# Kernel tuning notes

Measured on AMD Instinct MI355X. Metric: run time of the kernel, lower is better.

## Reference

```python
import jax, jax.numpy as jnp
import numpy as np

B, H, W, C = 2, 128, 128, 128
NS = 8                      # attn_num_splits
WH, WW = H // NS, W // NS   # window size 16x16
SH, SW = WH // 2, WW // 2   # shift sizes
HID = 2 * C * 4             # ffn hidden (in_channels = 2*d_model, expansion 4)
EPS = 1e-5


def _make_swin_mask():
    # Standard shifted-window attention mask: -100 between different regions.
    img = np.zeros((H, W), np.int32)
    cnt = 0
    for hs in (slice(0, -WH), slice(-WH, -SH), slice(-SH, None)):
        for ws in (slice(0, -WW), slice(-WW, -SW), slice(-SW, None)):
            img[hs, ws] = cnt
            cnt += 1
    ids = img.reshape(NS, WH, NS, WW).transpose(0, 2, 1, 3).reshape(NS * NS, WH * WW)
    mask = np.where(ids[:, None, :] != ids[:, :, None], -100.0, 0.0).astype(np.float32)
    return jnp.asarray(mask)  # (64, 256, 256)


def _layernorm(x, g, b):
    m = jnp.mean(x, axis=-1, keepdims=True)
    v = jnp.mean(jnp.square(x - m), axis=-1, keepdims=True)
    return (x - m) * jax.lax.rsqrt(v + EPS) * g + b


def setup_inputs() -> dict:
    key = jax.random.key(0)
    ks = jax.random.split(key, 8)
    s = 1.0 / np.sqrt(C)
    return {
        "source": jax.random.normal(ks[0], (B, H * W, C), jnp.float32),
        "target": jax.random.normal(ks[1], (B, H * W, C), jnp.float32),
        "Wq": jax.random.normal(ks[2], (C, C), jnp.float32) * s,
        "Wk": jax.random.normal(ks[3], (C, C), jnp.float32) * s,
        "Wv": jax.random.normal(ks[4], (C, C), jnp.float32) * s,
        "Wm": jax.random.normal(ks[5], (C, C), jnp.float32) * s,
        "g1": jnp.ones((C,), jnp.float32),
        "b1": jnp.zeros((C,), jnp.float32),
        "W1": jax.random.normal(ks[6], (2 * C, HID), jnp.float32) * (1.0 / np.sqrt(2 * C)),
        "W2": jax.random.normal(ks[7], (HID, C), jnp.float32) * (1.0 / np.sqrt(HID)),
        "g2": jnp.ones((C,), jnp.float32),
        "b2": jnp.zeros((C,), jnp.float32),
        "shifted_window_attn_mask": _make_swin_mask(),
        "height": H,
        "width": W,
        "attn_num_splits": NS,
    }


def reference(source, target, Wq, Wk, Wv, Wm, g1, b1, W1, W2, g2, b2,
              shifted_window_attn_mask, height, width, attn_num_splits):
    b, L, c = source.shape
    h, w, ns = height, width, attn_num_splits
    wh, ww = h // ns, w // ns
    sh, sw = wh // 2, ww // 2

    q = source @ Wq
    k = target @ Wk
    v = target @ Wv

    def to_windows(x):
        # (b, h*w, c) -> shifted -> (b, nWin, wh*ww, c)
        x = x.reshape(b, h, w, c)
        x = jnp.roll(x, (-sh, -sw), axis=(1, 2))
        x = x.reshape(b, ns, wh, ns, ww, c).transpose(0, 1, 3, 2, 4, 5)
        return x.reshape(b, ns * ns, wh * ww, c)

    qw, kw, vw = to_windows(q), to_windows(k), to_windows(v)
    scores = jnp.einsum('bnlc,bnmc->bnlm', qw, kw) / (c ** 0.5)
    scores = scores + shifted_window_attn_mask[None]  # broadcast over batch
    attn = jax.nn.softmax(scores, axis=-1)
    out = jnp.einsum('bnlm,bnmc->bnlc', attn, vw)

    # merge windows back and undo the shift
    out = out.reshape(b, ns, ns, wh, ww, c).transpose(0, 1, 3, 2, 4, 5).reshape(b, h, w, c)
    out = jnp.roll(out, (sh, sw), axis=(1, 2)).reshape(b, h * w, c)

    message = _layernorm(out @ Wm, g1, b1)
    ffn_in = jnp.concatenate([source, message], axis=-1)
    message = jax.nn.gelu(ffn_in @ W1, approximate=False) @ W2
    message = _layernorm(message, g2, b2)
    return source + message
```

## Files before the change

### kernel.cpp

```cpp
#include <hip/hip_runtime.h>
#include <math.h>
#include <stdint.h>


typedef unsigned short u16;
typedef __attribute__((ext_vector_type(8))) short bf16x8;
typedef __attribute__((ext_vector_type(4))) float f32x4;
typedef __attribute__((ext_vector_type(4))) short u16x4;
typedef __attribute__((ext_vector_type(2))) unsigned int u32x2;

__device__ __forceinline__ u16 f2b(float f) {
    unsigned int i = __float_as_uint(f);
    unsigned int r = (i + 0x7fffu + ((i >> 16) & 1u)) >> 16;
    return (u16)r;
}

__device__ __forceinline__ float gelu_e(float x) {
    float y = fabsf(x) * 0.70710678118f;
    float u = fmaf(y, fmaf(y, fmaf(y, fmaf(y, 0.078108f, 0.000972f),
                                   0.230389f), 0.278393f), 1.0f);
    u = u * u; u = u * u;
    float r = __builtin_amdgcn_rcpf(u);
    return fmaxf(x, 0.f) - 0.5f * fabsf(x) * r;
}

__device__ __forceinline__ void cp16(const void* g, void* l) {
    auto* gp = reinterpret_cast<const __attribute__((address_space(1))) unsigned int*>(
        reinterpret_cast<uintptr_t>(g));
    auto* lp = reinterpret_cast<__attribute__((address_space(3))) unsigned int*>(
        reinterpret_cast<uintptr_t>(l));
    __builtin_amdgcn_global_load_lds(gp, lp, 16, 0, 0);
}

__device__ __forceinline__ int win_map(int gm) {
    int b = gm >> 14, rr = gm & 16383;
    int win = rr >> 8, t = rr & 255;
    int wi = win >> 3, wj = win & 7, i = t >> 4, j = t & 15;
    int h = (wi * 16 + i + 8) & 127;
    int w = (wj * 16 + j + 8) & 127;
    return (b << 14) + h * 128 + w;
}

__global__ __launch_bounds__(256, 2)
void gemm_qkv(const u16* __restrict__ srcb, const u16* __restrict__ tgtb,
              const u16* __restrict__ Bt, u16* __restrict__ qw,
              u16* __restrict__ kw, u16* __restrict__ vwt)
{
    __shared__ __align__(16) u16 SMEM[32768];
    u16* As = SMEM;
    u16* Bs = SMEM + 16384;
    u16* Ts = SMEM;

    const int tid = threadIdx.x;
    const int w = tid >> 6, lane = tid & 63;
    const int lm = lane & 15, q = lane >> 4;
    const int wm = w >> 1, wn = w & 1;
    const int m0 = blockIdx.x * 128;
    const int y = blockIdx.y;
    const u16* Ab = (y == 0) ? srcb : tgtb;

#pragma unroll
    for (int s = 0; s < 4; ++s)
#pragma unroll
        for (int i = 0; i < 2; ++i) {
            int row = w * 32 + i * 16 + (lane >> 2);
            int kc = s * 32 + (lane & 3) * 8;
            cp16(Ab + (size_t)win_map(m0 + row) * 128 + kc,
                 (void*)(As + (s * 128 + w * 32 + i * 16) * 32));
            cp16(Bt + (size_t)(y * 128 + row) * 128 + kc,
                 (void*)(Bs + (s * 128 + w * 32 + i * 16) * 32));
        }
    __syncthreads();

    f32x4 acc[4][4] = {};
#pragma unroll
    for (int s = 0; s < 4; ++s) {
        bf16x8 af[4], bfr[4];
#pragma unroll
        for (int t = 0; t < 4; ++t)
            af[t] = *(const bf16x8*)(As + (s * 128 + wm * 64 + t * 16 + lm) * 32 + q * 8);
#pragma unroll
        for (int t = 0; t < 4; ++t)
            bfr[t] = *(const bf16x8*)(Bs + (s * 128 + wn * 64 + t * 16 + lm) * 32 + q * 8);
#pragma unroll
        for (int mt = 0; mt < 4; ++mt)
#pragma unroll
            for (int nt = 0; nt < 4; ++nt)
                acc[mt][nt] = __builtin_amdgcn_mfma_f32_16x16x32_bf16(
                    af[mt], bfr[nt], acc[mt][nt], 0, 0, 0);
    }

    __syncthreads();
#pragma unroll
    for (int mt = 0; mt < 4; ++mt)
#pragma unroll
        for (int nt = 0; nt < 4; ++nt)
#pragma unroll
            for (int r = 0; r < 4; ++r) {
                int rowl = wm * 64 + mt * 16 + q * 4 + r;
                int col = wn * 64 + nt * 16 + lm;
                int idx = (y == 2) ? col * 136 + rowl : rowl * 136 + col;
                Ts[idx] = f2b(acc[mt][nt][r]);
            }
    __syncthreads();
    const int c8 = (tid & 15) * 8;
#pragma unroll
    for (int i = 0; i < 8; ++i) {
        int rr = i * 16 + (tid >> 4);
        bf16x8 t = *(const bf16x8*)(Ts + rr * 136 + c8);
        if (y == 2) {
            int wix = m0 >> 8, tok0 = m0 & 255;
            *(bf16x8*)(vwt + (size_t)wix * 32768 + (size_t)rr * 256 + tok0 + c8) = t;
        } else {
            u16* Cv = (y == 0) ? qw : kw;
            *(bf16x8*)(Cv + (size_t)(m0 + rr) * 128 + c8) = t;
        }
    }
}

__global__ __launch_bounds__(256, 2)
void attn_msg(const u16* __restrict__ qw, const u16* __restrict__ kw,
              const u16* __restrict__ vt, const u16* __restrict__ wmt,
              const float* __restrict__ g, const float* __restrict__ bb,
              u16* __restrict__ msgb)
{
    __shared__ __align__(16) u16 Ps[64 * 264];
    __shared__ __align__(16) u16 B32[16384];

    const int tid = threadIdx.x, w = tid >> 6, lane = tid & 63;
    const int lm = lane & 15, q = lane >> 4;
    const int l4r = lane >> 2, l4c = (lane & 3) * 8;
    const int bid = blockIdx.x;
    const int qc = bid & 3, win = (bid >> 2) & 63, b = bid >> 8;
    const int wi = win >> 3, wj = win & 7;
    const int q0 = qc * 64;
    const size_t wbase = (size_t)(b * 64 + win);
    const u16* kwb = kw + wbase * 256 * 128;
    const u16* qwb = qw + wbase * 256 * 128;
    const u16* vtb = vt + wbase * 128 * 256;

    u16* Qs = Ps;
#pragma unroll
    for (int i = 0; i < 4; ++i)
        cp16(qwb + (size_t)(q0 + w * 16 + l4r) * 128 + i * 32 + l4c,
             (void*)(Qs + (i * 64 + w * 16) * 32));
#pragma unroll
    for (int s = 0; s < 4; ++s)
#pragma unroll
        for (int i = 0; i < 2; ++i) {
            int tok = w * 32 + i * 16 + l4r;
            cp16(kwb + (size_t)tok * 128 + s * 32 + l4c,
                 (void*)(B32 + (s * 128 + w * 32 + i * 16) * 32));
        }
    __syncthreads();

    bf16x8 af[4];
#pragma unroll
    for (int kt = 0; kt < 4; ++kt)
        af[kt] = *(const bf16x8*)(Qs + (kt * 64 + w * 16 + lm) * 32 + q * 8);

    f32x4 s[16];
#pragma unroll
    for (int nt = 0; nt < 16; ++nt) { f32x4 z = {0.f, 0.f, 0.f, 0.f}; s[nt] = z; }
#pragma unroll
    for (int kt = 0; kt < 4; ++kt)
#pragma unroll
        for (int nt = 0; nt < 8; ++nt) {
            bf16x8 bf = *(const bf16x8*)(B32 + (kt * 128 + nt * 16 + lm) * 32 + q * 8);
            s[nt] = __builtin_amdgcn_mfma_f32_16x16x32_bf16(af[kt], bf, s[nt], 0, 0, 0);
        }
    __syncthreads();
#pragma unroll
    for (int ss = 0; ss < 4; ++ss)
#pragma unroll
        for (int i = 0; i < 2; ++i) {
            int tok = 128 + w * 32 + i * 16 + l4r;
            cp16(kwb + (size_t)tok * 128 + ss * 32 + l4c,
                 (void*)(B32 + (ss * 128 + w * 32 + i * 16) * 32));
        }
    __syncthreads();
#pragma unroll
    for (int kt = 0; kt < 4; ++kt)
#pragma unroll
        for (int nt = 8; nt < 16; ++nt) {
            bf16x8 bf = *(const bf16x8*)(B32 + (kt * 128 + (nt - 8) * 16 + lm) * 32 + q * 8);
            s[nt] = __builtin_amdgcn_mfma_f32_16x16x32_bf16(af[kt], bf, s[nt], 0, 0, 0);
        }
    __syncthreads();

#pragma unroll
    for (int tt = 0; tt < 4; ++tt)
#pragma unroll
        for (int i = 0; i < 2; ++i) {
            int ch = w * 32 + i * 16 + l4r;
            cp16(vtb + (size_t)ch * 256 + tt * 32 + l4c,
                 (void*)(B32 + (tt * 128 + w * 32 + i * 16) * 32));
        }

    int idk[16];
#pragma unroll
    for (int nt = 0; nt < 16; ++nt) {
        int rh = (wi == 7) ? ((nt >= 8) ? 2 : 1) : 0;
        int rw = (wj == 7) ? ((lm >= 8) ? 2 : 1) : 0;
        idk[nt] = rh * 3 + rw;
    }
    const float scale = 0.08838834764831845f;
#pragma unroll
    for (int r = 0; r < 4; ++r) {
        int tq = q0 + w * 16 + q * 4 + r;
        int iq = tq >> 4, jq = tq & 15;
        int rhq = (wi == 7) ? ((iq >= 8) ? 2 : 1) : 0;
        int rwq = (wj == 7) ? ((jq >= 8) ? 2 : 1) : 0;
        int idq = rhq * 3 + rwq;
        float sv[16];
        float mx = -1e30f;
#pragma unroll
        for (int nt = 0; nt < 16; ++nt) {
            float x = s[nt][r] * scale + ((idq != idk[nt]) ? -100.f : 0.f);
            sv[nt] = x; mx = fmaxf(mx, x);
        }
        mx = fmaxf(mx, __shfl_xor(mx, 1));
        mx = fmaxf(mx, __shfl_xor(mx, 2));
        mx = fmaxf(mx, __shfl_xor(mx, 4));
        mx = fmaxf(mx, __shfl_xor(mx, 8));
        float sum = 0.f;
#pragma unroll
        for (int nt = 0; nt < 16; ++nt) { float e = __expf(sv[nt] - mx); sv[nt] = e; sum += e; }
        sum += __shfl_xor(sum, 1);
        sum += __shfl_xor(sum, 2);
        sum += __shfl_xor(sum, 4);
        sum += __shfl_xor(sum, 8);
        float inv = 1.0f / sum;
#pragma unroll
        for (int nt = 0; nt < 16; ++nt)
            Ps[(w * 16 + q * 4 + r) * 264 + nt * 16 + lm] = f2b(sv[nt] * inv);
    }
    __syncthreads();

    f32x4 o[8];
#pragma unroll
    for (int nt = 0; nt < 8; ++nt) { f32x4 z = {0.f, 0.f, 0.f, 0.f}; o[nt] = z; }
#pragma unroll
    for (int tt = 0; tt < 4; ++tt) {
        bf16x8 pf = *(const bf16x8*)(Ps + (w * 16 + lm) * 264 + tt * 32 + q * 8);
#pragma unroll
        for (int nt = 0; nt < 8; ++nt) {
            bf16x8 vf = *(const bf16x8*)(B32 + (tt * 128 + nt * 16 + lm) * 32 + q * 8);
            o[nt] = __builtin_amdgcn_mfma_f32_16x16x32_bf16(pf, vf, o[nt], 0, 0, 0);
        }
    }
    __syncthreads();
#pragma unroll
    for (int tt = 0; tt < 4; ++tt)
#pragma unroll
        for (int i = 0; i < 2; ++i) {
            int ch = w * 32 + i * 16 + l4r;
            cp16(vtb + (size_t)ch * 256 + 128 + tt * 32 + l4c,
                 (void*)(B32 + (tt * 128 + w * 32 + i * 16) * 32));
        }
    __syncthreads();
#pragma unroll
    for (int tt = 4; tt < 8; ++tt) {
        bf16x8 pf = *(const bf16x8*)(Ps + (w * 16 + lm) * 264 + tt * 32 + q * 8);
#pragma unroll
        for (int nt = 0; nt < 8; ++nt) {
            bf16x8 vf = *(const bf16x8*)(B32 + ((tt - 4) * 128 + nt * 16 + lm) * 32 + q * 8);
            o[nt] = __builtin_amdgcn_mfma_f32_16x16x32_bf16(pf, vf, o[nt], 0, 0, 0);
        }
    }
    __syncthreads();

#pragma unroll
    for (int ss = 0; ss < 4; ++ss)
#pragma unroll
        for (int i = 0; i < 2; ++i) {
            int n = w * 32 + i * 16 + l4r;
            cp16(wmt + (size_t)n * 128 + ss * 32 + l4c,
                 (void*)(B32 + (ss * 128 + w * 32 + i * 16) * 32));
        }
    u16* Ot = Ps;
#pragma unroll
    for (int r = 0; r < 4; ++r) {
        int rl = w * 16 + q * 4 + r;
#pragma unroll
        for (int nt = 0; nt < 8; ++nt)
            Ot[rl * 136 + nt * 16 + lm] = f2b(o[nt][r]);
    }
    __syncthreads();

    f32x4 macc[8];
#pragma unroll
    for (int n2 = 0; n2 < 8; ++n2) { f32x4 z = {0.f, 0.f, 0.f, 0.f}; macc[n2] = z; }
#pragma unroll
    for (int kt = 0; kt < 4; ++kt) {
        bf16x8 paf = *(const bf16x8*)(Ot + (w * 16 + lm) * 136 + kt * 32 + q * 8);
#pragma unroll
        for (int n2 = 0; n2 < 8; ++n2) {
            bf16x8 wf = *(const bf16x8*)(B32 + (kt * 128 + n2 * 16 + lm) * 32 + q * 8);
            macc[n2] = __builtin_amdgcn_mfma_f32_16x16x32_bf16(paf, wf, macc[n2], 0, 0, 0);
        }
    }

    float gv[8], bv[8];
#pragma unroll
    for (int n2 = 0; n2 < 8; ++n2) {
        int col = n2 * 16 + lm;
        gv[n2] = g[col]; bv[n2] = bb[col];
    }
#pragma unroll
    for (int r = 0; r < 4; ++r) {
        float s1 = 0.f, s2 = 0.f;
#pragma unroll
        for (int n2 = 0; n2 < 8; ++n2) {
            float v = macc[n2][r];
            s1 += v; s2 += v * v;
        }
        s1 += __shfl_xor(s1, 1); s2 += __shfl_xor(s2, 1);
        s1 += __shfl_xor(s1, 2); s2 += __shfl_xor(s2, 2);
        s1 += __shfl_xor(s1, 4); s2 += __shfl_xor(s2, 4);
        s1 += __shfl_xor(s1, 8); s2 += __shfl_xor(s2, 8);
        float mean = s1 * (1.f / 128.f);
        float var = fmaxf(s2 * (1.f / 128.f) - mean * mean, 0.f);
        float rs = rsqrtf(var + 1e-5f);
        int t = q0 + w * 16 + q * 4 + r;
        int ii = t >> 4, jj = t & 15;
        int h = (wi * 16 + ii + 8) & 127;
        int w2 = (wj * 16 + jj + 8) & 127;
        size_t orow = ((size_t)b * 16384 + h * 128 + w2) * 128;
#pragma unroll
        for (int n2 = 0; n2 < 8; ++n2)
            msgb[orow + n2 * 16 + lm] = f2b((macc[n2][r] - mean) * rs * gv[n2] + bv[n2]);
    }
}

__global__ __launch_bounds__(1024, 4)
void fused_ffn(const u16* __restrict__ A0, const u16* __restrict__ A1,
               const u16* __restrict__ W1T, const u16* __restrict__ W2T,
               const float* __restrict__ g, const float* __restrict__ bb,
               const float* __restrict__ resid, float* __restrict__ outv)
{
    __shared__ __align__(16) u16 W1s[32768];
    __shared__ __align__(16) u16 W2s[16384];
    __shared__ __align__(16) u16 Gs[8192];

    const int tid = threadIdx.x;
    const int w = tid >> 6, lane = tid & 63;
    const int lm = lane & 15, q = lane >> 4;
    const int l4r = lane >> 2, l4c = (lane & 3) * 8;
    const int wm = w >> 2, wn = w & 3;
    const int m0 = blockIdx.x * 128;

    const int s_ks = w >> 1, s_hh = (w & 1) * 32;
    const int s_s2 = w >> 3, s_rg = w & 7;

    bf16x8 areg[2][8];
#pragma unroll
    for (int mt = 0; mt < 2; ++mt)
#pragma unroll
        for (int ks = 0; ks < 8; ++ks) {
            const u16* Ab = (ks < 4) ? A0 : A1;
            areg[mt][ks] = *(const bf16x8*)(
                Ab + (size_t)(m0 + wm * 32 + mt * 16 + lm) * 128 + (ks & 3) * 32 + q * 8);
        }
#pragma unroll
    for (int i = 0; i < 2; ++i)
        cp16(W1T + (size_t)(s_hh + i * 16 + l4r) * 256 + s_ks * 32 + l4c,
             (void*)(W1s + (s_ks * 64 + s_hh + i * 16) * 32));
    cp16(W2T + (size_t)(s_rg * 16 + l4r) * 1024 + s_s2 * 32 + l4c,
         (void*)(W2s + (s_s2 * 128 + s_rg * 16) * 32));
    __syncthreads();

    f32x4 acc2[2][2] = {};
    for (int c = 0; c < 16; ++c) {
        const int cur = c & 1;
        const u16* W1c = W1s + cur * 16384;
        const u16* W2c = W2s + cur * 8192;
        if (c < 15) {
            u16* W1n = W1s + (cur ^ 1) * 16384;
            u16* W2n = W2s + (cur ^ 1) * 8192;
#pragma unroll
            for (int i = 0; i < 2; ++i)
                cp16(W1T + (size_t)((c + 1) * 64 + s_hh + i * 16 + l4r) * 256 + s_ks * 32 + l4c,
                     (void*)(W1n + (s_ks * 64 + s_hh + i * 16) * 32));
            cp16(W2T + (size_t)(s_rg * 16 + l4r) * 1024 + (c + 1) * 64 + s_s2 * 32 + l4c,
                 (void*)(W2n + (s_s2 * 128 + s_rg * 16) * 32));
        }
        f32x4 acc1[2] = {};
#pragma unroll
        for (int ks = 0; ks < 8; ++ks) {
            bf16x8 w1f = *(const bf16x8*)(W1c + (ks * 64 + wn * 16 + lm) * 32 + q * 8);
#pragma unroll
            for (int mt = 0; mt < 2; ++mt)
                acc1[mt] = __builtin_amdgcn_mfma_f32_16x16x32_bf16(
                    w1f, areg[mt][ks], acc1[mt], 0, 0, 0);
        }
#pragma unroll
        for (int mt = 0; mt < 2; ++mt) {
            float g0 = gelu_e(acc1[mt][0]), g1 = gelu_e(acc1[mt][1]);
            float g2 = gelu_e(acc1[mt][2]), g3 = gelu_e(acc1[mt][3]);
            unsigned p0, p1;
            asm("v_cvt_pk_bf16_f32 %0, %1, %2" : "=v"(p0) : "v"(g0), "v"(g1));
            asm("v_cvt_pk_bf16_f32 %0, %1, %2" : "=v"(p1) : "v"(g2), "v"(g3));
            int tok = wm * 32 + mt * 16 + lm;
            int slot = (wn * 2 + (q >> 1)) ^ (tok & 7);
            u32x2 pk; pk[0] = p0; pk[1] = p1;
            *(u32x2*)(Gs + tok * 64 + slot * 8 + (q & 1) * 4) = pk;
        }
        __syncthreads();
#pragma unroll
        for (int ks = 0; ks < 2; ++ks) {
            bf16x8 pa[2], wf[2];
#pragma unroll
            for (int mt = 0; mt < 2; ++mt) {
                int tok = wm * 32 + mt * 16 + lm;
                pa[mt] = *(const bf16x8*)(Gs + tok * 64 + (((ks * 4 + q) ^ (tok & 7)) * 8));
            }
#pragma unroll
            for (int nt = 0; nt < 2; ++nt)
                wf[nt] = *(const bf16x8*)(W2c + (ks * 128 + wn * 32 + nt * 16 + lm) * 32 + q * 8);
#pragma unroll
            for (int mt = 0; mt < 2; ++mt)
#pragma unroll
                for (int nt = 0; nt < 2; ++nt)
                    acc2[mt][nt] = __builtin_amdgcn_mfma_f32_16x16x32_bf16(
                        pa[mt], wf[nt], acc2[mt][nt], 0, 0, 0);
        }
        __syncthreads();
    }

    float* stats = (float*)Gs;
#pragma unroll
    for (int mt = 0; mt < 2; ++mt)
#pragma unroll
        for (int r = 0; r < 4; ++r) {
            float s1 = 0.f, s2 = 0.f;
#pragma unroll
            for (int nt = 0; nt < 2; ++nt) {
                float v = acc2[mt][nt][r];
                s1 += v; s2 += v * v;
            }
            s1 += __shfl_xor(s1, 1); s2 += __shfl_xor(s2, 1);
            s1 += __shfl_xor(s1, 2); s2 += __shfl_xor(s2, 2);
            s1 += __shfl_xor(s1, 4); s2 += __shfl_xor(s2, 4);
            s1 += __shfl_xor(s1, 8); s2 += __shfl_xor(s2, 8);
            if (lm == 0) {
                int row = wm * 32 + mt * 16 + q * 4 + r;
                stats[row * 8 + wn * 2] = s1;
                stats[row * 8 + wn * 2 + 1] = s2;
            }
        }
    __syncthreads();

    float gv[2], bv[2];
#pragma unroll
    for (int nt = 0; nt < 2; ++nt) {
        int col = wn * 32 + nt * 16 + lm;
        gv[nt] = g[col]; bv[nt] = bb[col];
    }
#pragma unroll
    for (int mt = 0; mt < 2; ++mt)
#pragma unroll
        for (int r = 0; r < 4; ++r) {
            int row = wm * 32 + mt * 16 + q * 4 + r;
            f32x4 st0 = *(const f32x4*)(stats + row * 8);
            f32x4 st1 = *(const f32x4*)(stats + row * 8 + 4);
            float s1 = st0[0] + st0[2] + st1[0] + st1[2];
            float s2 = st0[1] + st0[3] + st1[1] + st1[3];
            float mean = s1 * (1.f / 128.f);
            float var = fmaxf(s2 * (1.f / 128.f) - mean * mean, 0.f);
            float rs = rsqrtf(var + 1e-5f);
#pragma unroll
            for (int nt = 0; nt < 2; ++nt) {
                int col = wn * 32 + nt * 16 + lm;
                size_t gi = (size_t)(m0 + row) * 128 + col;
                outv[gi] = (acc2[mt][nt][r] - mean) * rs * gv[nt] + bv[nt] + resid[gi];
            }
        }
}

__global__ void prep_all(const float* __restrict__ Wq, const float* __restrict__ Wk,
                         const float* __restrict__ Wv, const float* __restrict__ Wm,
                         const float* __restrict__ W1, const float* __restrict__ W2,
                         const float* __restrict__ src, const float* __restrict__ tgt,
                         u16* __restrict__ ws, u16* __restrict__ srcb,
                         u16* __restrict__ tgtb)
{
    int bx = blockIdx.x;
    if (bx < 1792) {
        int idx = bx * 256 + threadIdx.x;
        if (idx < 65536) {
            int m = idx >> 14, e = idx & 16383;
            const float* sp = (m == 0) ? Wq : (m == 1) ? Wk : (m == 2) ? Wv : Wm;
            int n = e >> 7, k = e & 127;
            ws[m * 16384 + n * 128 + k] = f2b(sp[k * 128 + n]);
        } else if (idx < 327680) {
            int e = idx - 65536;
            int n = e >> 8, k = e & 255;
            ws[65536 + n * 256 + k] = f2b(W1[k * 1024 + n]);
        } else {
            int e = idx - 327680;
            int n = e >> 10, k = e & 1023;
            ws[327680 + n * 1024 + k] = f2b(W2[k * 128 + n]);
        }
    } else {
        int idx = (bx - 1792) * 256 + threadIdx.x;
        const float* s; u16* d; int i;
        if (idx < 1048576) { s = src; d = srcb; i = idx * 4; }
        else               { s = tgt; d = tgtb; i = (idx - 1048576) * 4; }
        f32x4 v = *(const f32x4*)(s + i);
        u16x4 o; o[0] = f2b(v[0]); o[1] = f2b(v[1]); o[2] = f2b(v[2]); o[3] = f2b(v[3]);
        *(u16x4*)(d + i) = o;
    }
}

#define OFF_WQT  0u
#define OFF_WMT  49152u
#define OFF_W1T  65536u
#define OFF_W2T  327680u
#define OFF_SRCB 458752u
#define OFF_TGTB 4653056u
#define OFF_QW   8847360u
#define OFF_KW   13041664u
#define OFF_VWT  17235968u
#define OFF_MSGB 21430272u

extern "C" void kernel_launch(void* const* d_in, const int* in_sizes, int n_in,
                              void* d_out, int out_size, void* d_ws, size_t ws_size,
                              hipStream_t stream)
{
    (void)in_sizes; (void)n_in; (void)out_size; (void)ws_size;
    const float* source = (const float*)d_in[0];
    const float* target = (const float*)d_in[1];
    const float* Wq = (const float*)d_in[2];
    const float* Wk = (const float*)d_in[3];
    const float* Wv = (const float*)d_in[4];
    const float* Wm = (const float*)d_in[5];
    const float* g1 = (const float*)d_in[6];
    const float* b1 = (const float*)d_in[7];
    const float* W1 = (const float*)d_in[8];
    const float* W2 = (const float*)d_in[9];
    const float* g2 = (const float*)d_in[10];
    const float* b2 = (const float*)d_in[11];
    u16* ws = (u16*)d_ws;
    float* out = (float*)d_out;

    prep_all<<<9984, 256, 0, stream>>>(Wq, Wk, Wv, Wm, W1, W2, source, target,
                                       ws, ws + OFF_SRCB, ws + OFF_TGTB);
    gemm_qkv<<<dim3(256, 3), 256, 0, stream>>>(
        ws + OFF_SRCB, ws + OFF_TGTB, ws + OFF_WQT,
        ws + OFF_QW, ws + OFF_KW, ws + OFF_VWT);
    attn_msg<<<512, 256, 0, stream>>>(
        ws + OFF_QW, ws + OFF_KW, ws + OFF_VWT, ws + OFF_WMT, g1, b1,
        ws + OFF_MSGB);
    fused_ffn<<<256, 1024, 0, stream>>>(
        ws + OFF_SRCB, ws + OFF_MSGB, ws + OFF_W1T, ws + OFF_W2T,
        g2, b2, source, out);
}
```

Baseline: 192.2 us.

## Software-pipeline FFN chunks: overlap GEMM1+GELU of next chunk with GEMM2

Restructures the fused FFN hidden-chunk loop so that GEMM1 and GELU for chunk c+1 run in the same iteration as GEMM2 for chunk c. The GELU staging buffer becomes double-buffered and the W1 prefetch runs two chunks ahead. This removes one __syncthreads per chunk and lets independent MFMA work interleave. In exchange it uses more LDS (Gs doubles, about 16KB more) and has a more complex buffer schedule, which could raise register pressure.

```diff
diff --git a/kernel.cpp b/kernel.cpp
--- a/kernel.cpp
+++ b/kernel.cpp
@@ -341,7 +341,7 @@
 {
     __shared__ __align__(16) u16 W1s[32768];
     __shared__ __align__(16) u16 W2s[16384];
-    __shared__ __align__(16) u16 Gs[8192];
+    __shared__ __align__(16) u16 Gs[16384];
 
     const int tid = threadIdx.x;
     const int w = tid >> 6, lane = tid & 63;
@@ -353,6 +353,13 @@
     const int s_ks = w >> 1, s_hh = (w & 1) * 32;
     const int s_s2 = w >> 3, s_rg = w & 7;
 
+    const u16* w1p = W1T + (size_t)(s_hh + l4r) * 256 + s_ks * 32 + l4c;
+    const u16* w2p = W2T + (size_t)(s_rg * 16 + l4r) * 1024 + s_s2 * 32 + l4c;
+    u16* const w1d0 = W1s + (s_ks * 64 + s_hh) * 32;
+    u16* const w1d1 = w1d0 + 16384;
+    u16* const w2d0 = W2s + (s_s2 * 128 + s_rg * 16) * 32;
+    u16* const w2d1 = w2d0 + 8192;
+
     bf16x8 areg[2][8];
 #pragma unroll
     for (int mt = 0; mt < 2; ++mt)
@@ -362,33 +369,19 @@
             areg[mt][ks] = *(const bf16x8*)(
                 Ab + (size_t)(m0 + wm * 32 + mt * 16 + lm) * 128 + (ks & 3) * 32 + q * 8);
         }
-#pragma unroll
-    for (int i = 0; i < 2; ++i)
-        cp16(W1T + (size_t)(s_hh + i * 16 + l4r) * 256 + s_ks * 32 + l4c,
-             (void*)(W1s + (s_ks * 64 + s_hh + i * 16) * 32));
-    cp16(W2T + (size_t)(s_rg * 16 + l4r) * 1024 + s_s2 * 32 + l4c,
-         (void*)(W2s + (s_s2 * 128 + s_rg * 16) * 32));
-    __syncthreads();
-
-    f32x4 acc2[2][2] = {};
-    for (int c = 0; c < 16; ++c) {
-        const int cur = c & 1;
-        const u16* W1c = W1s + cur * 16384;
-        const u16* W2c = W2s + cur * 8192;
-        if (c < 15) {
-            u16* W1n = W1s + (cur ^ 1) * 16384;
-            u16* W2n = W2s + (cur ^ 1) * 8192;
-#pragma unroll
-            for (int i = 0; i < 2; ++i)
-                cp16(W1T + (size_t)((c + 1) * 64 + s_hh + i * 16 + l4r) * 256 + s_ks * 32 + l4c,
-                     (void*)(W1n + (s_ks * 64 + s_hh + i * 16) * 32));
-            cp16(W2T + (size_t)(s_rg * 16 + l4r) * 1024 + (c + 1) * 64 + s_s2 * 32 + l4c,
-                 (void*)(W2n + (s_s2 * 128 + s_rg * 16) * 32));
-        }
+
+    cp16(w1p, w1d0); cp16(w1p + 16 * 256, w1d0 + 512);
+    cp16(w2p, w2d0);
+    w1p += 16384; w2p += 64;
+    __syncthreads();
+
+    cp16(w1p, w1d1); cp16(w1p + 16 * 256, w1d1 + 512);
+    w1p += 16384;
+    {
         f32x4 acc1[2] = {};
 #pragma unroll
         for (int ks = 0; ks < 8; ++ks) {
-            bf16x8 w1f = *(const bf16x8*)(W1c + (ks * 64 + wn * 16 + lm) * 32 + q * 8);
+            bf16x8 w1f = *(const bf16x8*)(W1s + (ks * 64 + wn * 16 + lm) * 32 + q * 8);
 #pragma unroll
             for (int mt = 0; mt < 2; ++mt)
                 acc1[mt] = __builtin_amdgcn_mfma_f32_16x16x32_bf16(
@@ -406,24 +399,70 @@
             u32x2 pk; pk[0] = p0; pk[1] = p1;
             *(u32x2*)(Gs + tok * 64 + slot * 8 + (q & 1) * 4) = pk;
         }
-        __syncthreads();
-#pragma unroll
-        for (int ks = 0; ks < 2; ++ks) {
-            bf16x8 pa[2], wf[2];
+    }
+    __syncthreads();
+
+    f32x4 acc2[2][2] = {};
+#pragma unroll 2
+    for (int c = 0; c < 16; ++c) {
+        const int cb = c & 1, nb = cb ^ 1;
+        if (c + 2 < 16) {
+            u16* d = cb ? w1d1 : w1d0;
+            cp16(w1p, d); cp16(w1p + 16 * 256, d + 512);
+        }
+        if (c + 1 < 16) {
+            u16* d = nb ? w2d1 : w2d0;
+            cp16(w2p, d);
+        }
+        w1p += 16384; w2p += 64;
+
+        if (c + 1 < 16) {
+            const u16* W1c = W1s + nb * 16384;
+            f32x4 acc1[2] = {};
+#pragma unroll
+            for (int ks = 0; ks < 8; ++ks) {
+                bf16x8 w1f = *(const bf16x8*)(W1c + (ks * 64 + wn * 16 + lm) * 32 + q * 8);
+#pragma unroll
+                for (int mt = 0; mt < 2; ++mt)
+                    acc1[mt] = __builtin_amdgcn_mfma_f32_16x16x32_bf16(
+                        w1f, areg[mt][ks], acc1[mt], 0, 0, 0);
+            }
+            u16* Gw = Gs + nb * 8192;
 #pragma unroll
             for (int mt = 0; mt < 2; ++mt) {
+                float g0 = gelu_e(acc1[mt][0]), g1 = gelu_e(acc1[mt][1]);
+                float g2 = gelu_e(acc1[mt][2]), g3 = gelu_e(acc1[mt][3]);
+                unsigned p0, p1;
+                asm("v_cvt_pk_bf16_f32 %0, %1, %2" : "=v"(p0) : "v"(g0), "v"(g1));
+                asm("v_cvt_pk_bf16_f32 %0, %1, %2" : "=v"(p1) : "v"(g2), "v"(g3));
                 int tok = wm * 32 + mt * 16 + lm;
-                pa[mt] = *(const bf16x8*)(Gs + tok * 64 + (((ks * 4 + q) ^ (tok & 7)) * 8));
-            }
-#pragma unroll
-            for (int nt = 0; nt < 2; ++nt)
-                wf[nt] = *(const bf16x8*)(W2c + (ks * 128 + wn * 32 + nt * 16 + lm) * 32 + q * 8);
-#pragma unroll
-            for (int mt = 0; mt < 2; ++mt)
+                int slot = (wn * 2 + (q >> 1)) ^ (tok & 7);
+                u32x2 pk; pk[0] = p0; pk[1] = p1;
+                *(u32x2*)(Gw + tok * 64 + slot * 8 + (q & 1) * 4) = pk;
+            }
+        }
+
+        {
+            const u16* W2c = W2s + cb * 8192;
+            const u16* Gr = Gs + cb * 8192;
+#pragma unroll
+            for (int ks = 0; ks < 2; ++ks) {
+                bf16x8 pa[2], wf[2];
+#pragma unroll
+                for (int mt = 0; mt < 2; ++mt) {
+                    int tok = wm * 32 + mt * 16 + lm;
+                    pa[mt] = *(const bf16x8*)(Gr + tok * 64 + (((ks * 4 + q) ^ (tok & 7)) * 8));
+                }
 #pragma unroll
                 for (int nt = 0; nt < 2; ++nt)
-                    acc2[mt][nt] = __builtin_amdgcn_mfma_f32_16x16x32_bf16(
-                        pa[mt], wf[nt], acc2[mt][nt], 0, 0, 0);
+                    wf[nt] = *(const bf16x8*)(W2c + (ks * 128 + wn * 32 + nt * 16 + lm) * 32 + q * 8);
+#pragma unroll
+                for (int mt = 0; mt < 2; ++mt)
+#pragma unroll
+                    for (int nt = 0; nt < 2; ++nt)
+                        acc2[mt][nt] = __builtin_amdgcn_mfma_f32_16x16x32_bf16(
+                            pa[mt], wf[nt], acc2[mt][nt], 0, 0, 0);
+            }
         }
         __syncthreads();
     }
```

Result: no change. 191.5 us (-0.4%).

## Halve FFN block tile to 64 tokens and single-buffer W1 chunk in LDS

Applied to the files above, without the earlier changes.

The fused FFN kernel now uses 512-thread blocks covering 64 tokens each, launched as 512 blocks instead of 256 blocks of 1024 threads. The W1 chunk is single-buffered: the next chunk is loaded after the barrier that follows the first GEMM, while W2 stays double-buffered. This halves W1 and G LDS use so more blocks can be resident and the grid spreads across more CUs. The cost is twice as many loads of the weight chunks per token, and the W1 load is now exposed to the GEMM2 phase rather than a full iteration.

```diff
diff --git a/kernel.cpp b/kernel.cpp
--- a/kernel.cpp
+++ b/kernel.cpp
@@ -333,25 +333,28 @@
     }
 }
 
-__global__ __launch_bounds__(1024, 4)
+__global__ __launch_bounds__(512, 4)
 void fused_ffn(const u16* __restrict__ A0, const u16* __restrict__ A1,
                const u16* __restrict__ W1T, const u16* __restrict__ W2T,
                const float* __restrict__ g, const float* __restrict__ bb,
                const float* __restrict__ resid, float* __restrict__ outv)
 {
-    __shared__ __align__(16) u16 W1s[32768];
+    __shared__ __align__(16) u16 W1s[16384];
     __shared__ __align__(16) u16 W2s[16384];
-    __shared__ __align__(16) u16 Gs[8192];
+    __shared__ __align__(16) u16 Gs[4096];
 
     const int tid = threadIdx.x;
     const int w = tid >> 6, lane = tid & 63;
     const int lm = lane & 15, q = lane >> 4;
     const int l4r = lane >> 2, l4c = (lane & 3) * 8;
     const int wm = w >> 2, wn = w & 3;
-    const int m0 = blockIdx.x * 128;
-
-    const int s_ks = w >> 1, s_hh = (w & 1) * 32;
-    const int s_s2 = w >> 3, s_rg = w & 7;
+    const int m0 = blockIdx.x * 64;
+
+    const u16* w1p = W1T + (size_t)l4r * 256 + w * 32 + l4c;
+    const u16* w2p = W2T + (size_t)((w & 3) * 32 + l4r) * 1024 + (w >> 2) * 32 + l4c;
+    u16* const w1d = W1s + (w * 64) * 32;
+    u16* const w2d0 = W2s + (((w >> 2) * 128 + (w & 3) * 32)) * 32;
+    u16* const w2d1 = w2d0 + 8192;
 
     bf16x8 areg[2][8];
 #pragma unroll
@@ -362,68 +365,77 @@
             areg[mt][ks] = *(const bf16x8*)(
                 Ab + (size_t)(m0 + wm * 32 + mt * 16 + lm) * 128 + (ks & 3) * 32 + q * 8);
         }
+
+#pragma unroll
+    for (int i = 0; i < 4; ++i)
+        cp16(w1p + (size_t)(i * 16) * 256, w1d + (i * 16) * 32);
 #pragma unroll
     for (int i = 0; i < 2; ++i)
-        cp16(W1T + (size_t)(s_hh + i * 16 + l4r) * 256 + s_ks * 32 + l4c,
-             (void*)(W1s + (s_ks * 64 + s_hh + i * 16) * 32));
-    cp16(W2T + (size_t)(s_rg * 16 + l4r) * 1024 + s_s2 * 32 + l4c,
-         (void*)(W2s + (s_s2 * 128 + s_rg * 16) * 32));
+        cp16(w2p + (size_t)(i * 16) * 1024, w2d0 + (i * 16) * 32);
+    w1p += 16384; w2p += 64;
     __syncthreads();
 
     f32x4 acc2[2][2] = {};
+#pragma unroll 2
     for (int c = 0; c < 16; ++c) {
-        const int cur = c & 1;
-        const u16* W1c = W1s + cur * 16384;
-        const u16* W2c = W2s + cur * 8192;
-        if (c < 15) {
-            u16* W1n = W1s + (cur ^ 1) * 16384;
-            u16* W2n = W2s + (cur ^ 1) * 8192;
+        const int cb = c & 1, nb = cb ^ 1;
+
+        {
+            f32x4 acc1[2] = {};
+#pragma unroll
+            for (int ks = 0; ks < 8; ++ks) {
+                bf16x8 w1f = *(const bf16x8*)(W1s + (ks * 64 + wn * 16 + lm) * 32 + q * 8);
+#pragma unroll
+                for (int mt = 0; mt < 2; ++mt)
+                    acc1[mt] = __builtin_amdgcn_mfma_f32_16x16x32_bf16(
+                        w1f, areg[mt][ks], acc1[mt], 0, 0, 0);
+            }
+#pragma unroll
+            for (int mt = 0; mt < 2; ++mt) {
+                float g0 = gelu_e(acc1[mt][0]), g1 = gelu_e(acc1[mt][1]);
+                float g2 = gelu_e(acc1[mt][2]), g3 = gelu_e(acc1[mt][3]);
+                unsigned p0, p1;
+                asm("v_cvt_pk_bf16_f32 %0, %1, %2" : "=v"(p0) : "v"(g0), "v"(g1));
+                asm("v_cvt_pk_bf16_f32 %0, %1, %2" : "=v"(p1) : "v"(g2), "v"(g3));
+                int tok = wm * 32 + mt * 16 + lm;
+                int slot = (wn * 2 + (q >> 1)) ^ (tok & 7);
+                u32x2 pk; pk[0] = p0; pk[1] = p1;
+                *(u32x2*)(Gs + tok * 64 + slot * 8 + (q & 1) * 4) = pk;
+            }
+        }
+        __syncthreads();
+
+        if (c + 1 < 16) {
+#pragma unroll
+            for (int i = 0; i < 4; ++i)
+                cp16(w1p + (size_t)(i * 16) * 256, w1d + (i * 16) * 32);
+            u16* d = nb ? w2d1 : w2d0;
 #pragma unroll
             for (int i = 0; i < 2; ++i)
-                cp16(W1T + (size_t)((c + 1) * 64 + s_hh + i * 16 + l4r) * 256 + s_ks * 32 + l4c,
-                     (void*)(W1n + (s_ks * 64 + s_hh + i * 16) * 32));
-            cp16(W2T + (size_t)(s_rg * 16 + l4r) * 1024 + (c + 1) * 64 + s_s2 * 32 + l4c,
-                 (void*)(W2n + (s_s2 * 128 + s_rg * 16) * 32));
-        }
-        f32x4 acc1[2] = {};
-#pragma unroll
-        for (int ks = 0; ks < 8; ++ks) {
-            bf16x8 w1f = *(const bf16x8*)(W1c + (ks * 64 + wn * 16 + lm) * 32 + q * 8);
-#pragma unroll
-            for (int mt = 0; mt < 2; ++mt)
-                acc1[mt] = __builtin_amdgcn_mfma_f32_16x16x32_bf16(
-                    w1f, areg[mt][ks], acc1[mt], 0, 0, 0);
-        }
-#pragma unroll
-        for (int mt = 0; mt < 2; ++mt) {
-            float g0 = gelu_e(acc1[mt][0]), g1 = gelu_e(acc1[mt][1]);
-            float g2 = gelu_e(acc1[mt][2]), g3 = gelu_e(acc1[mt][3]);
-            unsigned p0, p1;
-            asm("v_cvt_pk_bf16_f32 %0, %1, %2" : "=v"(p0) : "v"(g0), "v"(g1));
-            asm("v_cvt_pk_bf16_f32 %0, %1, %2" : "=v"(p1) : "v"(g2), "v"(g3));
-            int tok = wm * 32 + mt * 16 + lm;
-            int slot = (wn * 2 + (q >> 1)) ^ (tok & 7);
-            u32x2 pk; pk[0] = p0; pk[1] = p1;
-            *(u32x2*)(Gs + tok * 64 + slot * 8 + (q & 1) * 4) = pk;
-        }
-        __syncthreads();
-#pragma unroll
-        for (int ks = 0; ks < 2; ++ks) {
-            bf16x8 pa[2], wf[2];
-#pragma unroll
-            for (int mt = 0; mt < 2; ++mt) {
-                int tok = wm * 32 + mt * 16 + lm;
-                pa[mt] = *(const bf16x8*)(Gs + tok * 64 + (((ks * 4 + q) ^ (tok & 7)) * 8));
-            }
-#pragma unroll
-            for (int nt = 0; nt < 2; ++nt)
-                wf[nt] = *(const bf16x8*)(W2c + (ks * 128 + wn * 32 + nt * 16 + lm) * 32 + q * 8);
-#pragma unroll
-            for (int mt = 0; mt < 2; ++mt)
+                cp16(w2p + (size_t)(i * 16) * 1024, d + (i * 16) * 32);
+        }
+        w1p += 16384; w2p += 64;
+
+        {
+            const u16* W2c = W2s + cb * 8192;
+#pragma unroll
+            for (int ks = 0; ks < 2; ++ks) {
+                bf16x8 pa[2], wf[2];
+#pragma unroll
+                for (int mt = 0; mt < 2; ++mt) {
+                    int tok = wm * 32 + mt * 16 + lm;
+                    pa[mt] = *(const bf16x8*)(Gs + tok * 64 + (((ks * 4 + q) ^ (tok & 7)) * 8));
+                }
 #pragma unroll
                 for (int nt = 0; nt < 2; ++nt)
-                    acc2[mt][nt] = __builtin_amdgcn_mfma_f32_16x16x32_bf16(
-                        pa[mt], wf[nt], acc2[mt][nt], 0, 0, 0);
+                    wf[nt] = *(const bf16x8*)(W2c + (ks * 128 + wn * 32 + nt * 16 + lm) * 32 + q * 8);
+#pragma unroll
+                for (int mt = 0; mt < 2; ++mt)
+#pragma unroll
+                    for (int nt = 0; nt < 2; ++nt)
+                        acc2[mt][nt] = __builtin_amdgcn_mfma_f32_16x16x32_bf16(
+                            pa[mt], wf[nt], acc2[mt][nt], 0, 0, 0);
+            }
         }
         __syncthreads();
     }
@@ -552,7 +564,7 @@
     attn_msg<<<512, 256, 0, stream>>>(
         ws + OFF_QW, ws + OFF_KW, ws + OFF_VWT, ws + OFF_WMT, g1, b1,
         ws + OFF_MSGB);
-    fused_ffn<<<256, 1024, 0, stream>>>(
+    fused_ffn<<<512, 512, 0, stream>>>(
         ws + OFF_SRCB, ws + OFF_MSGB, ws + OFF_W1T, ws + OFF_W2T,
         g2, b2, source, out);
 }
```

Measured after the change: 196.2 us. 2.1% more time.
